# Kernel optimization log

Hardware: AMD Instinct MI355X
Metric: run time of the kernel (lower is better)

## Reference

```python
import jax, jax.numpy as jnp
import numpy as np

D_MODEL = 2048
NUM_HEADS = 16
D_K = D_MODEL // NUM_HEADS


def setup_inputs() -> dict:
    key = jax.random.key(0)
    ks = jax.random.split(key, 12)
    B, S, D = 2, 2048, D_MODEL
    s = 1.0 / np.sqrt(D)
    return {
        "q": jax.random.normal(ks[0], (B, S, D), jnp.float32),
        "k": jax.random.normal(ks[1], (B, S, D), jnp.float32),
        "v": jax.random.normal(ks[2], (B, S, D), jnp.float32),
        "Wq": jax.random.normal(ks[3], (D, D), jnp.float32) * s,
        "bq": jax.random.normal(ks[4], (D,), jnp.float32) * 0.01,
        "Wk": jax.random.normal(ks[5], (D, D), jnp.float32) * s,
        "bk": jax.random.normal(ks[6], (D,), jnp.float32) * 0.01,
        "Wv": jax.random.normal(ks[7], (D, D), jnp.float32) * s,
        "bv": jax.random.normal(ks[8], (D,), jnp.float32) * 0.01,
        "Wo": jax.random.normal(ks[9], (D, D), jnp.float32) * s,
        "bo": jax.random.normal(ks[10], (D,), jnp.float32) * 0.01,
    }


def reference(q, k, v, Wq, bq, Wk, bk, Wv, bv, Wo, bo):
    B, S, D = q.shape
    H, dk = NUM_HEADS, D_K

    def proj(x, W, b):
        # Linear then split heads -> [B, H, S, dk]
        y = jnp.einsum('bsd,df->bsf', x, W) + b
        return y.reshape(B, -1, H, dk).transpose(0, 2, 1, 3)

    Q = proj(q, Wq, bq)
    K = proj(k, Wk, bk)
    V = proj(v, Wv, bv)

    scores = jnp.einsum('bhqd,bhkd->bhqk', Q, K) / jnp.sqrt(jnp.float32(dk))
    attn = jax.nn.softmax(scores, axis=-1)  # dropout is identity (eval)
    out = jnp.einsum('bhqk,bhkd->bhqd', attn, V)
    out = out.transpose(0, 2, 1, 3).reshape(B, -1, D)
    return jnp.einsum('bsd,df->bsf', out, Wo) + bo
```

## Files before the change

kernel.cpp:

```cpp
#include <hip/hip_runtime.h>
#include <hip/hip_bf16.h>
#include <stdint.h>

typedef float  f32x4  __attribute__((ext_vector_type(4)));
typedef float  f32x16 __attribute__((ext_vector_type(16)));
typedef short  s16x8  __attribute__((ext_vector_type(8)));

#define D_MODEL 2048
#define NHEADS  16
#define DK      128
#define BATCH   2
#define SEQ     2048
#define MROWS   (BATCH*SEQ)

__device__ __forceinline__ unsigned short f2bf(float f) {
  union { float f; unsigned int u; } v; v.f = f;
  unsigned int r = v.u + 0x7FFFu + ((v.u >> 16) & 1u);
  return (unsigned short)(r >> 16);
}

__device__ __forceinline__ unsigned int packbf_c(float lo, float hi) {
  __hip_bfloat16 l = __float2bfloat16(lo);
  __hip_bfloat16 h = __float2bfloat16(hi);
  unsigned short lu, hu;
  __builtin_memcpy(&lu, &l, 2);
  __builtin_memcpy(&hu, &h, 2);
  return (unsigned int)lu | ((unsigned int)hu << 16);
}

__device__ __forceinline__ void async16(const void* g, void* l) {
  __builtin_amdgcn_global_load_lds(
      (const __attribute__((address_space(1))) unsigned int*)g,
      (__attribute__((address_space(3))) unsigned int*)l,
      16, 0, 0);
}

__global__ __launch_bounds__(256) void f2b3_kernel(const float* __restrict__ q,
                                                   const float* __restrict__ k,
                                                   const float* __restrict__ v,
                                                   unsigned short* __restrict__ qb,
                                                   unsigned short* __restrict__ kb,
                                                   unsigned short* __restrict__ vb) {
  const float* s; unsigned short* d;
  switch (blockIdx.y) {
    case 0:  s = q; d = qb; break;
    case 1:  s = k; d = kb; break;
    default: s = v; d = vb; break;
  }
  int i = blockIdx.x * 256 + threadIdx.x;
  const float4* s4 = (const float4*)s;
  float4 a = s4[2*i];
  float4 b = s4[2*i+1];
  s16x8 o;
  o[0] = (short)f2bf(a.x); o[1] = (short)f2bf(a.y);
  o[2] = (short)f2bf(a.z); o[3] = (short)f2bf(a.w);
  o[4] = (short)f2bf(b.x); o[5] = (short)f2bf(b.y);
  o[6] = (short)f2bf(b.z); o[7] = (short)f2bf(b.w);
  *(s16x8*)(d + 8*(size_t)i) = o;
}

__global__ __launch_bounds__(256) void wtrans_kernel(const float* __restrict__ Wq,
                                                     const float* __restrict__ Wk,
                                                     const float* __restrict__ Wv,
                                                     const float* __restrict__ Wo,
                                                     unsigned short* __restrict__ WqT,
                                                     unsigned short* __restrict__ WkT,
                                                     unsigned short* __restrict__ WvT,
                                                     unsigned short* __restrict__ WoT) {
  const float* W; unsigned short* Wt;
  switch (blockIdx.z) {
    case 0:  W = Wq; Wt = WqT; break;
    case 1:  W = Wk; Wt = WkT; break;
    case 2:  W = Wv; Wt = WvT; break;
    default: W = Wo; Wt = WoT; break;
  }
  __shared__ float tl[32][33];
  int x = threadIdx.x, y = threadIdx.y;
  int n0 = blockIdx.x * 32, k0 = blockIdx.y * 32;
  #pragma unroll
  for (int j = 0; j < 32; j += 8)
    tl[y + j][x] = W[(size_t)(k0 + y + j) * D_MODEL + n0 + x];
  __syncthreads();
  #pragma unroll
  for (int j = 0; j < 32; j += 8)
    Wt[(size_t)(n0 + y + j) * D_MODEL + k0 + x] = f2bf(tl[x][y + j]);
}

__device__ __forceinline__ void gemm_core(const unsigned short* __restrict__ A,
                                          const unsigned short* __restrict__ Bt,
                                          const float* __restrict__ bias,
                                          void* __restrict__ Cout,
                                          int M, int N, int K,
                                          int mode, float scale,
                                          int m0, int n0,
                                          unsigned short* As0, unsigned short* As1,
                                          unsigned short* Bs0, unsigned short* Bs1) {
  const int t  = threadIdx.x;
  const int l  = t & 63, w = t >> 6;
  const int wr = w >> 1, wc = w & 1;
  const int lr = l & 15, lg = l >> 4;

  unsigned short* Asb[2] = {As0, As1};
  unsigned short* Bsb[2] = {Bs0, Bs1};

  const int c0row = t >> 2, c0col = (t & 3) * 8;
  const int c1row = (t + 256) >> 2, c1col = ((t + 256) & 3) * 8;

  async16(A  + (size_t)(m0 + c0row)*K + c0col, (char*)As0 + t*16);
  async16(Bt + (size_t)(n0 + c0row)*K + c0col, (char*)Bs0 + t*16);
  async16(A  + (size_t)(m0 + c1row)*K + c1col, (char*)As0 + (t+256)*16);
  async16(Bt + (size_t)(n0 + c1row)*K + c1col, (char*)Bs0 + (t+256)*16);
  asm volatile("s_waitcnt vmcnt(0)" ::: "memory");
  __syncthreads();

  f32x4 acc[4][4] = {};

  for (int k0 = 0; k0 < K; k0 += 32) {
    const int cur = (k0 >> 5) & 1;
    if (k0 + 32 < K) {
      const int kn = k0 + 32;
      async16(A  + (size_t)(m0 + c0row)*K + kn + c0col, (char*)Asb[cur^1] + t*16);
      async16(Bt + (size_t)(n0 + c0row)*K + kn + c0col, (char*)Bsb[cur^1] + t*16);
      async16(A  + (size_t)(m0 + c1row)*K + kn + c1col, (char*)Asb[cur^1] + (t+256)*16);
      async16(Bt + (size_t)(n0 + c1row)*K + kn + c1col, (char*)Bsb[cur^1] + (t+256)*16);
    }

    s16x8 af[4], bfr[4];
    #pragma unroll
    for (int m = 0; m < 4; ++m)
      af[m] = *(const s16x8*)&Asb[cur][(wr*64 + m*16 + lr)*32 + 8*lg];
    #pragma unroll
    for (int n = 0; n < 4; ++n)
      bfr[n] = *(const s16x8*)&Bsb[cur][(wc*64 + n*16 + lr)*32 + 8*lg];
    #pragma unroll
    for (int m = 0; m < 4; ++m)
      #pragma unroll
      for (int n = 0; n < 4; ++n)
        acc[m][n] = __builtin_amdgcn_mfma_f32_16x16x32_bf16(af[m], bfr[n], acc[m][n], 0, 0, 0);

    asm volatile("s_waitcnt vmcnt(0)" ::: "memory");
    __syncthreads();
  }

  if (mode == 0) {
    float* C = (float*)Cout;
    #pragma unroll
    for (int n = 0; n < 4; ++n) {
      int col = n0 + wc*64 + n*16 + lr;
      float bv = bias[col];
      #pragma unroll
      for (int m = 0; m < 4; ++m) {
        int rowb = m0 + wr*64 + m*16 + lg*4;
        #pragma unroll
        for (int r = 0; r < 4; ++r)
          C[(size_t)(rowb + r)*N + col] = (acc[m][n][r] + bv) * scale;
      }
    }
  } else {
    unsigned short* C = (unsigned short*)Cout;
    #pragma unroll
    for (int n = 0; n < 4; ++n) {
      int col = n0 + wc*64 + n*16 + lr;
      float bv = bias[col];
      int h = col >> 7, dkk = col & 127;
      #pragma unroll
      for (int m = 0; m < 4; ++m) {
        int rowb = m0 + wr*64 + m*16 + lg*4;
        #pragma unroll
        for (int r = 0; r < 4; ++r) {
          int row = rowb + r;
          int b = row >> 11, s = row & 2047;
          C[((size_t)((b*NHEADS + h)*SEQ + s))*DK + dkk] = f2bf((acc[m][n][r] + bv) * scale);
        }
      }
    }
  }
}

__global__ __launch_bounds__(256) void gemm_bt(const unsigned short* __restrict__ A,
                                               const unsigned short* __restrict__ Bt,
                                               const float* __restrict__ bias,
                                               void* __restrict__ Cout,
                                               int M, int N, int K,
                                               int mode, float scale) {
  __shared__ unsigned short As[2][128*32];
  __shared__ unsigned short Bs[2][128*32];
  gemm_core(A, Bt, bias, Cout, M, N, K, mode, scale,
            blockIdx.y*128, blockIdx.x*128, As[0], As[1], Bs[0], Bs[1]);
}

__global__ __launch_bounds__(256) void gemm_qkv3(const unsigned short* __restrict__ qb,
                                                 const unsigned short* __restrict__ kb,
                                                 const unsigned short* __restrict__ vb,
                                                 const unsigned short* __restrict__ WT,
                                                 const float* __restrict__ bq,
                                                 const float* __restrict__ bk,
                                                 const float* __restrict__ bv,
                                                 unsigned short* __restrict__ Hout,
                                                 float qscale) {
  __shared__ unsigned short As[2][128*32];
  __shared__ unsigned short Bs[2][128*32];
  const int z = blockIdx.z;
  const unsigned short* A = (z == 0) ? qb : (z == 1) ? kb : vb;
  const float* bias       = (z == 0) ? bq : (z == 1) ? bk : bv;
  const float scale       = (z == 0) ? qscale : 1.0f;
  const unsigned short* Bt = WT + (size_t)z * D_MODEL * D_MODEL;
  unsigned short* Cout     = Hout + (size_t)z * MROWS * D_MODEL;
  gemm_core(A, Bt, bias, Cout, MROWS, D_MODEL, D_MODEL, 1, scale,
            blockIdx.y*128, blockIdx.x*128, As[0], As[1], Bs[0], Bs[1]);
}

__global__ __launch_bounds__(256, 2) void attn_kernel(const unsigned short* __restrict__ Q,
                                                      const unsigned short* __restrict__ K,
                                                      const unsigned short* __restrict__ V,
                                                      unsigned short* __restrict__ O) {
  __shared__ char lds[64*256 + 128*144];
  unsigned short* Kl = (unsigned short*)lds;
  unsigned short* Vt = (unsigned short*)(lds + 64*256);

  const int t  = threadIdx.x;
  const int l  = t & 63, w = t >> 6;
  const int q_ = l & 31, hi = l >> 5;
  const int bh = blockIdx.y;
  const int b  = bh >> 4, h = bh & 15;
  const int q0 = blockIdx.x * 128;

  const unsigned short* Qp = Q + (size_t)bh * SEQ * DK;
  const unsigned short* Kp = K + (size_t)bh * SEQ * DK;
  const unsigned short* Vp = V + (size_t)bh * SEQ * DK;

  const int qrow = q0 + w*32 + q_;
  s16x8 aq[8];
  #pragma unroll
  for (int kk = 0; kk < 8; ++kk)
    aq[kk] = *(const s16x8*)(Qp + (size_t)qrow*DK + kk*16 + hi*8);

  f32x16 accO[4] = {};
  float m = -INFINITY, L = 0.f;

  const int vp_ = t & 31;
  const int vd0 = (t >> 5) * 8;

  for (int kv0 = 0; kv0 < SEQ; kv0 += 64) {
    __syncthreads();
    #pragma unroll
    for (int i = 0; i < 4; ++i) {
      int c   = t + 256*i;
      int row = c >> 4;
      int sb  = ((c & 15) << 4) ^ ((row & 15) << 4);
      async16((const char*)(Kp + (size_t)(kv0 + row)*DK) + sb, (char*)Kl + c*16);
    }
    #pragma unroll
    for (int rep = 0; rep < 2; ++rep) {
      int dvb = vd0 + rep*64;
      s16x8 va = *(const s16x8*)(Vp + (size_t)(kv0 + 2*vp_    )*DK + dvb);
      s16x8 vb = *(const s16x8*)(Vp + (size_t)(kv0 + 2*vp_ + 1)*DK + dvb);
      #pragma unroll
      for (int j = 0; j < 8; ++j) {
        unsigned int pk = (unsigned int)(unsigned short)va[j]
                        | ((unsigned int)(unsigned short)vb[j] << 16);
        *(unsigned int*)&Vt[(dvb + j)*72 + 2*vp_] = pk;
      }
    }
    asm volatile("s_waitcnt vmcnt(0) lgkmcnt(0)" ::: "memory");
    __syncthreads();

    f32x16 S0 = {}, S1 = {};
    #pragma unroll
    for (int t2 = 0; t2 < 2; ++t2) {
      int krow = t2*32 + q_;
      const char* kb = (const char*)Kl + krow*256;
      int swz = (krow & 15) << 4;
      #pragma unroll
      for (int kk = 0; kk < 8; ++kk) {
        s16x8 kf = *(const s16x8*)(kb + ((kk*32 + hi*16) ^ swz));
        if (t2 == 0) S0 = __builtin_amdgcn_mfma_f32_32x32x16_bf16(kf, aq[kk], S0, 0, 0, 0);
        else         S1 = __builtin_amdgcn_mfma_f32_32x32x16_bf16(kf, aq[kk], S1, 0, 0, 0);
      }
    }

    f32x16 mx;
    #pragma unroll
    for (int r = 0; r < 16; ++r) mx[r] = fmaxf(S0[r], S1[r]);
    float m8_[8];
    #pragma unroll
    for (int r = 0; r < 8; ++r) m8_[r] = fmaxf(mx[r], mx[r+8]);
    float m4a = fmaxf(m8_[0], m8_[4]), m4b = fmaxf(m8_[1], m8_[5]);
    float m4c = fmaxf(m8_[2], m8_[6]), m4d = fmaxf(m8_[3], m8_[7]);
    float pmax = fmaxf(fmaxf(m4a, m4b), fmaxf(m4c, m4d));
    pmax = fmaxf(pmax, __shfl_xor(pmax, 32, 64));

    if (!__all(pmax <= m + 11.0f)) {
      float mnew = fmaxf(m, pmax);
      float corr = exp2f(m - mnew);
      m = mnew;
      L *= corr;
      #pragma unroll
      for (int sub = 0; sub < 4; ++sub)
        #pragma unroll
        for (int r = 0; r < 16; ++r) accO[sub][r] *= corr;
    }

    float rs0 = 0.f, rs1 = 0.f, rs2 = 0.f, rs3 = 0.f;
    #pragma unroll
    for (int r = 0; r < 4; ++r) {
      float a0 = exp2f(S0[r]    - m); S0[r]    = a0; rs0 += a0;
      float a1 = exp2f(S0[r+4]  - m); S0[r+4]  = a1; rs1 += a1;
      float a2 = exp2f(S0[r+8]  - m); S0[r+8]  = a2; rs2 += a2;
      float a3 = exp2f(S0[r+12] - m); S0[r+12] = a3; rs3 += a3;
      float b0 = exp2f(S1[r]    - m); S1[r]    = b0; rs0 += b0;
      float b1 = exp2f(S1[r+4]  - m); S1[r+4]  = b1; rs1 += b1;
      float b2 = exp2f(S1[r+8]  - m); S1[r+8]  = b2; rs2 += b2;
      float b3 = exp2f(S1[r+12] - m); S1[r+12] = b3; rs3 += b3;
    }
    float rs = (rs0 + rs1) + (rs2 + rs3);
    rs += __shfl_xor(rs, 32, 64);
    L += rs;

    s16x8 PB[4];
    #pragma unroll
    for (int t2 = 0; t2 < 2; ++t2) {
      #pragma unroll
      for (int half = 0; half < 2; ++half) {
        int bse = half*8;
        unsigned int pkA01, pkA23, pkB01, pkB23;
        if (t2 == 0) {
          pkA01 = packbf_c(S0[bse+0], S0[bse+1]);
          pkA23 = packbf_c(S0[bse+2], S0[bse+3]);
          pkB01 = packbf_c(S0[bse+4], S0[bse+5]);
          pkB23 = packbf_c(S0[bse+6], S0[bse+7]);
        } else {
          pkA01 = packbf_c(S1[bse+0], S1[bse+1]);
          pkA23 = packbf_c(S1[bse+2], S1[bse+3]);
          pkB01 = packbf_c(S1[bse+4], S1[bse+5]);
          pkB23 = packbf_c(S1[bse+6], S1[bse+7]);
        }
        unsigned int xA01 = __shfl_xor(pkA01, 32, 64);
        unsigned int xA23 = __shfl_xor(pkA23, 32, 64);
        unsigned int xB01 = __shfl_xor(pkB01, 32, 64);
        unsigned int xB23 = __shfl_xor(pkB23, 32, 64);
        union { unsigned int u[4]; s16x8 v; } f;
        f.u[0] = hi ? xB01 : pkA01;
        f.u[1] = hi ? xB23 : pkA23;
        f.u[2] = hi ? pkB01 : xA01;
        f.u[3] = hi ? pkB23 : xA23;
        PB[t2*2 + half] = f.v;
      }
    }

    #pragma unroll
    for (int sub = 0; sub < 4; ++sub) {
      const char* vb2 = (const char*)Vt + (size_t)(sub*32 + q_)*144 + hi*16;
      #pragma unroll
      for (int kk = 0; kk < 4; ++kk) {
        s16x8 vf = *(const s16x8*)(vb2 + kk*32);
        accO[sub] = __builtin_amdgcn_mfma_f32_32x32x16_bf16(vf, PB[kk], accO[sub], 0, 0, 0);
      }
    }
  }

  __syncthreads();
  unsigned short* Ob = (unsigned short*)lds + (size_t)w*4096;
  float inv = 1.0f / L;
  #pragma unroll
  for (int sub = 0; sub < 4; ++sub)
    #pragma unroll
    for (int j = 0; j < 8; ++j) {
      unsigned int pw = packbf_c(accO[sub][2*j]*inv, accO[sub][2*j+1]*inv);
      int dv = sub*32 + (j&1)*2 + ((j>>1)*8) + 4*hi;
      *(unsigned int*)((char*)Ob + q_*256 + ((dv*2) ^ ((q_ & 15) << 4))) = pw;
    }
  asm volatile("s_waitcnt lgkmcnt(0)" ::: "memory");
  size_t gbase = ((size_t)(b*SEQ + q0 + w*32 + q_))*D_MODEL + h*DK;
  #pragma unroll
  for (int p = 0; p < 8; ++p) {
    int chunk = hi + 2*p;
    s16x8 ov = *(const s16x8*)((char*)Ob + q_*256 + ((chunk*16) ^ ((q_ & 15) << 4)));
    *(s16x8*)(O + gbase + chunk*8) = ov;
  }
}

extern "C" void kernel_launch(void* const* d_in, const int* in_sizes, int n_in,
                              void* d_out, int out_size, void* d_ws, size_t ws_size,
                              hipStream_t stream) {
  const float* q  = (const float*)d_in[0];
  const float* k  = (const float*)d_in[1];
  const float* v  = (const float*)d_in[2];
  const float* Wq = (const float*)d_in[3];
  const float* bq = (const float*)d_in[4];
  const float* Wk = (const float*)d_in[5];
  const float* bk = (const float*)d_in[6];
  const float* Wv = (const float*)d_in[7];
  const float* bv = (const float*)d_in[8];
  const float* Wo = (const float*)d_in[9];
  const float* bo = (const float*)d_in[10];
  float* out = (float*)d_out;

  char* ws = (char*)d_ws;
  const size_t SZT = (size_t)MROWS * D_MODEL * 2;
  const size_t SZW = (size_t)D_MODEL * D_MODEL * 2;

  unsigned short* qb  = (unsigned short*)(ws);
  unsigned short* kb  = (unsigned short*)(ws + SZT);
  unsigned short* vb  = (unsigned short*)(ws + 2*SZT);
  unsigned short* WqT = (unsigned short*)(ws + 3*SZT);
  unsigned short* WkT = (unsigned short*)(ws + 3*SZT + SZW);
  unsigned short* WvT = (unsigned short*)(ws + 3*SZT + 2*SZW);
  unsigned short* WoT = (unsigned short*)(ws + 3*SZT + 3*SZW);
  unsigned short* Qh  = (unsigned short*)(ws + 3*SZT + 4*SZW);
  unsigned short* Kh  = (unsigned short*)(ws + 4*SZT + 4*SZW);
  unsigned short* Vh  = (unsigned short*)(ws + 5*SZT + 4*SZW);
  unsigned short* Oc  = qb;

  const int n8 = MROWS * D_MODEL / 8;
  f2b3_kernel<<<dim3(n8/256, 3), 256, 0, stream>>>(q, k, v, qb, kb, vb);
  wtrans_kernel<<<dim3(64, 64, 4), dim3(32, 8), 0, stream>>>(Wq, Wk, Wv, Wo, WqT, WkT, WvT, WoT);

  const float qscale = 0.1275174308f;
  gemm_qkv3<<<dim3(16, 32, 3), 256, 0, stream>>>(qb, kb, vb, WqT, bq, bk, bv, Qh, qscale);

  attn_kernel<<<dim3(SEQ/128, BATCH*NHEADS), 256, 0, stream>>>(Qh, Kh, Vh, Oc);

  gemm_bt<<<dim3(16, 32), 256, 0, stream>>>(Oc, WoT, bo, out, MROWS, D_MODEL, D_MODEL, 0, 1.0f);
}
```

Before: 371.9 us.

## Rewrite projection GEMMs with 128x256 tiles, BK=64 and swizzled LDS

The QKV and output projection GEMMs now use a 512-thread block computing a 128x256 tile with a K-step of 64. LDS rows are XOR-swizzled to avoid bank conflicts, and loads are issued two stages ahead with partial vmcnt waits plus raw barriers. MFMA sections are wrapped in setprio. The aim is more data reuse per LDS byte, fewer bank conflicts and better latency hiding, at the cost of 96KB of LDS per block, which limits occupancy.

```diff
diff --git a/kernel.cpp b/kernel.cpp
--- a/kernel.cpp
+++ b/kernel.cpp
@@ -86,128 +86,146 @@
     Wt[(size_t)(n0 + y + j) * D_MODEL + k0 + x] = f2bf(tl[x][y + j]);
 }
 
-__device__ __forceinline__ void gemm_core(const unsigned short* __restrict__ A,
-                                          const unsigned short* __restrict__ Bt,
-                                          const float* __restrict__ bias,
-                                          void* __restrict__ Cout,
-                                          int M, int N, int K,
-                                          int mode, float scale,
-                                          int m0, int n0,
-                                          unsigned short* As0, unsigned short* As1,
-                                          unsigned short* Bs0, unsigned short* Bs1) {
+__device__ __forceinline__ void gemm256_core(const unsigned short* __restrict__ A,
+                                             const unsigned short* __restrict__ Bt,
+                                             const float* __restrict__ bias,
+                                             void* __restrict__ Cout,
+                                             int N, int K, int mode, float scale,
+                                             int m0, int n0, unsigned short* lds) {
   const int t  = threadIdx.x;
   const int l  = t & 63, w = t >> 6;
-  const int wr = w >> 1, wc = w & 1;
+  const int wm = w >> 2, wn = w & 3;
   const int lr = l & 15, lg = l >> 4;
 
-  unsigned short* Asb[2] = {As0, As1};
-  unsigned short* Bsb[2] = {Bs0, Bs1};
-
-  const int c0row = t >> 2, c0col = (t & 3) * 8;
-  const int c1row = (t + 256) >> 2, c1col = ((t + 256) & 3) * 8;
-
-  async16(A  + (size_t)(m0 + c0row)*K + c0col, (char*)As0 + t*16);
-  async16(Bt + (size_t)(n0 + c0row)*K + c0col, (char*)Bs0 + t*16);
-  async16(A  + (size_t)(m0 + c1row)*K + c1col, (char*)As0 + (t+256)*16);
-  async16(Bt + (size_t)(n0 + c1row)*K + c1col, (char*)Bs0 + (t+256)*16);
-  asm volatile("s_waitcnt vmcnt(0)" ::: "memory");
-  __syncthreads();
+  unsigned short* Ab[2] = { lds,         lds + 24576 };
+  unsigned short* Bb[2] = { lds + 8192,  lds + 24576 + 8192 };
+
+  auto STAGE = [&](int buf, int kt) {
+    unsigned short* Ad = Ab[buf];
+    unsigned short* Bd = Bb[buf];
+    #pragma unroll
+    for (int i = 0; i < 2; ++i) {
+      int c = t + 512*i;
+      int row = c >> 3, crs = (c & 7) ^ (row & 7);
+      async16(A + (size_t)(m0 + row)*K + kt*64 + crs*8, (char*)Ad + c*16);
+    }
+    #pragma unroll
+    for (int i = 0; i < 4; ++i) {
+      int c = t + 512*i;
+      int row = c >> 3, crs = (c & 7) ^ (row & 7);
+      async16(Bt + (size_t)(n0 + row)*K + kt*64 + crs*8, (char*)Bd + c*16);
+    }
+  };
+
+  const int NT = K >> 6;
+  STAGE(0, 0);
+  STAGE(1, 1);
+  asm volatile("s_waitcnt vmcnt(6)" ::: "memory");
+  __builtin_amdgcn_s_barrier();
 
   f32x4 acc[4][4] = {};
 
-  for (int k0 = 0; k0 < K; k0 += 32) {
-    const int cur = (k0 >> 5) & 1;
-    if (k0 + 32 < K) {
-      const int kn = k0 + 32;
-      async16(A  + (size_t)(m0 + c0row)*K + kn + c0col, (char*)Asb[cur^1] + t*16);
-      async16(Bt + (size_t)(n0 + c0row)*K + kn + c0col, (char*)Bsb[cur^1] + t*16);
-      async16(A  + (size_t)(m0 + c1row)*K + kn + c1col, (char*)Asb[cur^1] + (t+256)*16);
-      async16(Bt + (size_t)(n0 + c1row)*K + kn + c1col, (char*)Bsb[cur^1] + (t+256)*16);
-    }
-
-    s16x8 af[4], bfr[4];
-    #pragma unroll
-    for (int m = 0; m < 4; ++m)
-      af[m] = *(const s16x8*)&Asb[cur][(wr*64 + m*16 + lr)*32 + 8*lg];
-    #pragma unroll
-    for (int n = 0; n < 4; ++n)
-      bfr[n] = *(const s16x8*)&Bsb[cur][(wc*64 + n*16 + lr)*32 + 8*lg];
-    #pragma unroll
-    for (int m = 0; m < 4; ++m)
-      #pragma unroll
-      for (int n = 0; n < 4; ++n)
-        acc[m][n] = __builtin_amdgcn_mfma_f32_16x16x32_bf16(af[m], bfr[n], acc[m][n], 0, 0, 0);
-
-    asm volatile("s_waitcnt vmcnt(0)" ::: "memory");
-    __syncthreads();
+  for (int kt = 0; kt < NT; ++kt) {
+    const int cur = kt & 1;
+    const unsigned short* Ac = Ab[cur];
+    const unsigned short* Bc = Bb[cur];
+
+    #pragma unroll
+    for (int ks = 0; ks < 2; ++ks) {
+      const int cb = ks*64 + lg*16;
+      s16x8 af[4], bf[4];
+      #pragma unroll
+      for (int mf = 0; mf < 4; ++mf) {
+        int row = wm*64 + mf*16 + lr;
+        af[mf] = *(const s16x8*)((const char*)Ac + row*128 + (cb ^ ((row & 7) << 4)));
+      }
+      #pragma unroll
+      for (int nf = 0; nf < 4; ++nf) {
+        int row = wn*64 + nf*16 + lr;
+        bf[nf] = *(const s16x8*)((const char*)Bc + row*128 + (cb ^ ((row & 7) << 4)));
+      }
+      __builtin_amdgcn_s_setprio(1);
+      #pragma unroll
+      for (int mf = 0; mf < 4; ++mf)
+        #pragma unroll
+        for (int nf = 0; nf < 4; ++nf)
+          acc[mf][nf] = __builtin_amdgcn_mfma_f32_16x16x32_bf16(af[mf], bf[nf], acc[mf][nf], 0, 0, 0);
+      __builtin_amdgcn_s_setprio(0);
+    }
+
+    asm volatile("" ::: "memory");
+    __builtin_amdgcn_s_barrier();
+    if (kt + 2 < NT) {
+      STAGE(cur, kt + 2);
+      asm volatile("s_waitcnt vmcnt(6)" ::: "memory");
+    } else {
+      asm volatile("s_waitcnt vmcnt(0)" ::: "memory");
+    }
+    __builtin_amdgcn_s_barrier();
   }
 
   if (mode == 0) {
     float* C = (float*)Cout;
     #pragma unroll
-    for (int n = 0; n < 4; ++n) {
-      int col = n0 + wc*64 + n*16 + lr;
+    for (int nf = 0; nf < 4; ++nf) {
+      int col = n0 + wn*64 + nf*16 + lr;
       float bv = bias[col];
       #pragma unroll
-      for (int m = 0; m < 4; ++m) {
-        int rowb = m0 + wr*64 + m*16 + lg*4;
+      for (int mf = 0; mf < 4; ++mf) {
+        int rowb = m0 + wm*64 + mf*16 + lg*4;
         #pragma unroll
         for (int r = 0; r < 4; ++r)
-          C[(size_t)(rowb + r)*N + col] = (acc[m][n][r] + bv) * scale;
+          C[(size_t)(rowb + r)*N + col] = (acc[mf][nf][r] + bv) * scale;
       }
     }
   } else {
     unsigned short* C = (unsigned short*)Cout;
     #pragma unroll
-    for (int n = 0; n < 4; ++n) {
-      int col = n0 + wc*64 + n*16 + lr;
+    for (int nf = 0; nf < 4; ++nf) {
+      int col = n0 + wn*64 + nf*16 + lr;
       float bv = bias[col];
       int h = col >> 7, dkk = col & 127;
       #pragma unroll
-      for (int m = 0; m < 4; ++m) {
-        int rowb = m0 + wr*64 + m*16 + lg*4;
+      for (int mf = 0; mf < 4; ++mf) {
+        int rowb = m0 + wm*64 + mf*16 + lg*4;
         #pragma unroll
         for (int r = 0; r < 4; ++r) {
           int row = rowb + r;
           int b = row >> 11, s = row & 2047;
-          C[((size_t)((b*NHEADS + h)*SEQ + s))*DK + dkk] = f2bf((acc[m][n][r] + bv) * scale);
+          C[((size_t)((b*NHEADS + h)*SEQ + s))*DK + dkk] = f2bf((acc[mf][nf][r] + bv) * scale);
         }
       }
     }
   }
 }
 
-__global__ __launch_bounds__(256) void gemm_bt(const unsigned short* __restrict__ A,
-                                               const unsigned short* __restrict__ Bt,
-                                               const float* __restrict__ bias,
-                                               void* __restrict__ Cout,
-                                               int M, int N, int K,
-                                               int mode, float scale) {
-  __shared__ unsigned short As[2][128*32];
-  __shared__ unsigned short Bs[2][128*32];
-  gemm_core(A, Bt, bias, Cout, M, N, K, mode, scale,
-            blockIdx.y*128, blockIdx.x*128, As[0], As[1], Bs[0], Bs[1]);
-}
-
-__global__ __launch_bounds__(256) void gemm_qkv3(const unsigned short* __restrict__ qb,
-                                                 const unsigned short* __restrict__ kb,
-                                                 const unsigned short* __restrict__ vb,
-                                                 const unsigned short* __restrict__ WT,
-                                                 const float* __restrict__ bq,
-                                                 const float* __restrict__ bk,
-                                                 const float* __restrict__ bv,
-                                                 unsigned short* __restrict__ Hout,
-                                                 float qscale) {
-  __shared__ unsigned short As[2][128*32];
-  __shared__ unsigned short Bs[2][128*32];
+__global__ __launch_bounds__(512) void gemm256_qkv(const unsigned short* __restrict__ qb,
+                                                   const unsigned short* __restrict__ kb,
+                                                   const unsigned short* __restrict__ vb,
+                                                   const unsigned short* __restrict__ WT,
+                                                   const float* __restrict__ bq,
+                                                   const float* __restrict__ bk,
+                                                   const float* __restrict__ bv,
+                                                   unsigned short* __restrict__ Hout,
+                                                   float qscale) {
+  __shared__ unsigned short lds[49152];
   const int z = blockIdx.z;
   const unsigned short* A = (z == 0) ? qb : (z == 1) ? kb : vb;
   const float* bias       = (z == 0) ? bq : (z == 1) ? bk : bv;
   const float scale       = (z == 0) ? qscale : 1.0f;
   const unsigned short* Bt = WT + (size_t)z * D_MODEL * D_MODEL;
   unsigned short* Cout     = Hout + (size_t)z * MROWS * D_MODEL;
-  gemm_core(A, Bt, bias, Cout, MROWS, D_MODEL, D_MODEL, 1, scale,
-            blockIdx.y*128, blockIdx.x*128, As[0], As[1], Bs[0], Bs[1]);
+  gemm256_core(A, Bt, bias, Cout, D_MODEL, D_MODEL, 1, scale,
+               blockIdx.y*128, blockIdx.x*256, lds);
+}
+
+__global__ __launch_bounds__(512) void gemm256_out(const unsigned short* __restrict__ A,
+                                                   const unsigned short* __restrict__ Bt,
+                                                   const float* __restrict__ bias,
+                                                   float* __restrict__ Cout) {
+  __shared__ unsigned short lds[49152];
+  gemm256_core(A, Bt, bias, Cout, D_MODEL, D_MODEL, 0, 1.0f,
+               blockIdx.y*128, blockIdx.x*256, lds);
 }
 
 __global__ __launch_bounds__(256, 2) void attn_kernel(const unsigned short* __restrict__ Q,
@@ -417,9 +435,9 @@
   wtrans_kernel<<<dim3(64, 64, 4), dim3(32, 8), 0, stream>>>(Wq, Wk, Wv, Wo, WqT, WkT, WvT, WoT);
 
   const float qscale = 0.1275174308f;
-  gemm_qkv3<<<dim3(16, 32, 3), 256, 0, stream>>>(qb, kb, vb, WqT, bq, bk, bv, Qh, qscale);
+  gemm256_qkv<<<dim3(D_MODEL/256, MROWS/128, 3), 512, 0, stream>>>(qb, kb, vb, WqT, bq, bk, bv, Qh, qscale);
 
   attn_kernel<<<dim3(SEQ/128, BATCH*NHEADS), 256, 0, stream>>>(Qh, Kh, Vh, Oc);
 
-  gemm_bt<<<dim3(16, 32), 256, 0, stream>>>(Oc, WoT, bo, out, MROWS, D_MODEL, D_MODEL, 0, 1.0f);
-}
+  gemm256_out<<<dim3(D_MODEL/256, MROWS/128), 512, 0, stream>>>(Oc, WoT, bo, out);
+}
```

Result: slower. 383.3 us (+3.1%).
